# Kernel tuning notes

Hardware: AMD Instinct MI355X
Metric: run time of the kernel (lower is better)

## Reference

```python
import jax, jax.numpy as jnp
import numpy as np

BLOCK = 64          # block_dim
GAPS = (1, 64)      # block_dim**i for i in range(num_layers=2), input_dim=4096
N_BLOCKS = 64       # input_dim // block_dim
HID = 128           # 2 * block_dim (hidden_layers_ratio=[2])
BS = 8192
IN_DIM = 4096


def setup_inputs() -> dict:
    key = jax.random.key(0)
    kx, kw1, kw2 = jax.random.split(key, 3)
    x = jax.random.normal(kx, (BS, IN_DIM), dtype=jnp.float32)
    # one BlockResMLP per factorized layer: BlockLinear(64, 64, 128) -> ELU -> BlockLinear(64, 128, 64)
    w1 = jax.random.normal(kw1, (len(GAPS), N_BLOCKS, BLOCK, HID), dtype=jnp.float32) / np.sqrt(BLOCK)
    b1 = jnp.zeros((len(GAPS), N_BLOCKS, 1, HID), dtype=jnp.float32)
    w2 = jax.random.normal(kw2, (len(GAPS), N_BLOCKS, HID, BLOCK), dtype=jnp.float32) / np.sqrt(HID)
    b2 = jnp.zeros((len(GAPS), N_BLOCKS, 1, BLOCK), dtype=jnp.float32)
    return {"x": x, "w1": w1, "b1": b1, "w2": w2, "b2": b2}


def _facto(y, w1, b1, w2, b2):
    # BlockResMLP.forward: view(bs, n_blocks, BLOCK).transpose(0,1) -> batched block GEMMs -> residual
    bs = y.shape[0]
    z = y.reshape(bs, -1, BLOCK).transpose(1, 0, 2)              # (n_blocks, bs, BLOCK)
    h = jnp.einsum('nbd,nde->nbe', z, w1) + b1                   # BlockLinear 1 + bias
    h = jax.nn.elu(h)                                            # ELU (alpha=1)
    h = jnp.einsum('nbe,ned->nbd', h, w2) + b2                   # BlockLinear 2 + bias
    z = h + z                                                    # residual
    return z.transpose(1, 0, 2).reshape(bs, -1)


def reference(x, w1, b1, w2, b2):
    bs = x.shape[0]
    y = x
    for i, gap in enumerate(GAPS):
        # permutation shuffle: view(-1, BLOCK, gap).transpose(2,1).contiguous().view(bs,-1)
        y = y.reshape(-1, BLOCK, gap).transpose(0, 2, 1).reshape(bs, -1)
        y = _facto(y, w1[i], b1[i], w2[i], b2[i])
        # inverse shuffle: view(-1, gap, BLOCK).transpose(2,1)
        y = y.reshape(-1, gap, BLOCK).transpose(0, 2, 1).reshape(bs, -1)
    return y
```

## Files before the change

kernel.cpp:

```cpp
#include <hip/hip_runtime.h>


typedef short short8 __attribute__((ext_vector_type(8)));
typedef short short4v __attribute__((ext_vector_type(4)));
typedef float floatx4 __attribute__((ext_vector_type(4)));
typedef unsigned int uintx4 __attribute__((ext_vector_type(4)));

#define MFMA(A, B, C) __builtin_amdgcn_mfma_f32_16x16x32_bf16((A), (B), (C), 0, 0, 0)

__device__ __forceinline__ unsigned short bf16r(float f) {
  unsigned int u = __builtin_bit_cast(unsigned int, f);
  u += 0x7FFFu + ((u >> 16) & 1u);
  return (unsigned short)(u >> 16);
}
__device__ __forceinline__ float bf16f(unsigned short h) {
  unsigned int u = ((unsigned int)h) << 16;
  return __builtin_bit_cast(float, u);
}
__device__ __forceinline__ unsigned int pk2(float lo, float hi) {
  return (unsigned int)bf16r(lo) | ((unsigned int)bf16r(hi) << 16);
}
__device__ __forceinline__ float eluf(float v) {
  return v > 0.f ? v : (__expf(v) - 1.f);
}
__device__ __forceinline__ uint4 gather44(const short* A, const short* B, int s) {
  uint4 o;
  o.x = (unsigned int)(unsigned short)A[0 * s] |
        ((unsigned int)(unsigned short)A[1 * s] << 16);
  o.y = (unsigned int)(unsigned short)A[2 * s] |
        ((unsigned int)(unsigned short)A[3 * s] << 16);
  o.z = (unsigned int)(unsigned short)B[0 * s] |
        ((unsigned int)(unsigned short)B[1 * s] << 16);
  o.w = (unsigned int)(unsigned short)B[2 * s] |
        ((unsigned int)(unsigned short)B[3 * s] << 16);
  return o;
}

__global__ __launch_bounds__(256) void k0_prep(const float* __restrict__ w1,
                                               const float* __restrict__ w2,
                                               short* __restrict__ w1t,
                                               short* __restrict__ w2t) {
  __shared__ __align__(16) short T[128 * 72];
  const int t  = threadIdx.x;
  const int ln = blockIdx.x >> 1;
  if ((blockIdx.x & 1) == 0) {
    const bool pm = (ln >= 64);
    const float* src = w1 + (size_t)ln * 8192 + t * 32;
    const int d = t >> 2, e0 = (t & 3) * 32;
#pragma unroll
    for (int u = 0; u < 32; u += 2) {
      *(unsigned int*)&T[d * 136 + e0 + u] = pk2(src[u], src[u + 1]);
    }
    __syncthreads();
    const int e = t >> 1, d0 = (t & 1) * 32;
    short* dst = w1t + (size_t)ln * 8192 + e * 64 + d0;
#pragma unroll
    for (int k = 0; k < 4; ++k) {
      const int ta = d0 + (pm ? 4 * k : 8 * k);
      const int tb = d0 + (pm ? 16 + 4 * k : 8 * k + 4);
      *(uint4*)(dst + k * 8) = gather44(&T[ta * 136 + e], &T[tb * 136 + e], 136);
    }
  } else {
    const float* src = w2 + (size_t)ln * 8192 + t * 32;
    const int e = t >> 1, d0 = (t & 1) * 32;
#pragma unroll
    for (int u = 0; u < 32; u += 2) {
      *(unsigned int*)&T[e * 72 + d0 + u] = pk2(src[u], src[u + 1]);
    }
    __syncthreads();
    const int dp = t >> 2, e0 = (t & 3) * 32;
    short* dst = w2t + (size_t)ln * 8192 + dp * 128 + e0;
#pragma unroll
    for (int k = 0; k < 4; ++k) {
      const int ta = e0 + 4 * k;
      const int tb = e0 + 16 + 4 * k;
      *(uint4*)(dst + k * 8) = gather44(&T[ta * 72 + dp], &T[tb * 72 + dp], 72);
    }
  }
}

__global__ __launch_bounds__(256) void k1_layer0(
    const float* __restrict__ x,
    const short* __restrict__ w1t, const short* __restrict__ w2t,
    const float* __restrict__ b1,  const float* __restrict__ b2,
    short* __restrict__ y1) {
  const int tid  = threadIdx.x;
  const int lane = tid & 63;
  const int wv   = tid >> 6;
  const int il   = lane & 15;
  const int q    = lane >> 4;
  const int npair   = blockIdx.x & 31;
  const int rowtile = blockIdx.x >> 5;
  const int n  = npair * 2 + (wv & 1);
  const int r0 = rowtile * 64 + (wv >> 1) * 32;

  const short* w1n = w1t + (size_t)n * 8192;
  const short* w2n = w2t + (size_t)n * 8192;
  const float* b1n = b1 + n * 128;
  const float* b2n = b2 + n * 64;

  const floatx4 zero4 = {0.f, 0.f, 0.f, 0.f};
  short8 pbH;
#pragma unroll
  for (int v = 0; v < 8; ++v) pbH[v] = (v < 4 && il == q * 4 + v) ? (short)0x3F80 : (short)0;

  short8 a[2][2];
#pragma unroll
  for (int Mt = 0; Mt < 2; ++Mt) {
#pragma unroll
    for (int ks = 0; ks < 2; ++ks) {
      const float* xp = x + (size_t)(r0 + Mt * 16 + il) * 4096 + n * 64 + ks * 32 + q * 8;
      floatx4 f0 = *(const floatx4*)xp;
      floatx4 f1 = *(const floatx4*)(xp + 4);
      short8 t;
#pragma unroll
      for (int u = 0; u < 4; ++u) { t[u] = (short)bf16r(f0[u]); t[4 + u] = (short)bf16r(f1[u]); }
      a[ks][Mt] = t;
    }
  }

  floatx4 acc2[2][4] = {};
  for (int hh = 0; hh < 2; ++hh) {
    floatx4 acc1[2][4] = {};
#pragma unroll
    for (int ks = 0; ks < 2; ++ks) {
#pragma unroll
      for (int nt = 0; nt < 4; ++nt) {
        short8 b = *(const short8*)(w1n + (hh * 64 + nt * 16 + il) * 64 + ks * 32 + q * 8);
        acc1[0][nt] = MFMA(a[ks][0], b, acc1[0][nt]);
        acc1[1][nt] = MFMA(a[ks][1], b, acc1[1][nt]);
      }
    }
    uintx4 a2w[2][2];
#pragma unroll
    for (int Mt = 0; Mt < 2; ++Mt) {
#pragma unroll
      for (int nt = 0; nt < 4; ++nt) {
        const float bias = b1n[hh * 64 + nt * 16 + il];
        short8 ha = {(short)bf16r(eluf(acc1[Mt][nt][0] + bias)),
                     (short)bf16r(eluf(acc1[Mt][nt][1] + bias)),
                     (short)bf16r(eluf(acc1[Mt][nt][2] + bias)),
                     (short)bf16r(eluf(acc1[Mt][nt][3] + bias)),
                     0, 0, 0, 0};
        floatx4 hd = MFMA(ha, pbH, zero4);
        const int ks2l = nt >> 1;
        const int hf   = nt & 1;
        a2w[Mt][ks2l][hf * 2 + 0] = pk2(hd[0], hd[1]);
        a2w[Mt][ks2l][hf * 2 + 1] = pk2(hd[2], hd[3]);
      }
    }
#pragma unroll
    for (int ks2l = 0; ks2l < 2; ++ks2l) {
      short8 af0 = __builtin_bit_cast(short8, a2w[0][ks2l]);
      short8 af1 = __builtin_bit_cast(short8, a2w[1][ks2l]);
#pragma unroll
      for (int nt2 = 0; nt2 < 4; ++nt2) {
        short8 b = *(const short8*)(w2n + (nt2 * 16 + il) * 128 + hh * 64 + ks2l * 32 + q * 8);
        acc2[0][nt2] = MFMA(af0, b, acc2[0][nt2]);
        acc2[1][nt2] = MFMA(af1, b, acc2[1][nt2]);
      }
    }
  }

  short8 pb0, pb1;
#pragma unroll
  for (int v = 0; v < 8; ++v) {
    pb0[v] = (q * 8 + v == il)      ? (short)0x3F80 : (short)0;
    pb1[v] = (q * 8 + v == il + 16) ? (short)0x3F80 : (short)0;
  }
#pragma unroll
  for (int Mt = 0; Mt < 2; ++Mt) {
    const size_t nbase = ((size_t)((r0 + Mt * 16) >> 4) * 64 + n) * 64;
#pragma unroll
    for (int ks = 0; ks < 2; ++ks) {
      floatx4 xr[2];
      xr[0] = MFMA(a[ks][Mt], pb0, zero4);
      xr[1] = MFMA(a[ks][Mt], pb1, zero4);
#pragma unroll
      for (int h = 0; h < 2; ++h) {
        const int nt2 = ks * 2 + h;
        const int j = nt2 * 16 + il;
        const float bias = b2n[j];
        uint2 pk;
        pk.x = pk2(acc2[Mt][nt2][0] + bias + xr[h][0],
                   acc2[Mt][nt2][1] + bias + xr[h][1]);
        pk.y = pk2(acc2[Mt][nt2][2] + bias + xr[h][2],
                   acc2[Mt][nt2][3] + bias + xr[h][3]);
        *(uint2*)(y1 + (nbase + j) * 16 + q * 4) = pk;
      }
    }
  }
}

#define RSTR 1156
#define ISTR 18
__global__ __launch_bounds__(1024) void k2_layer1_out(
    const short* __restrict__ y1,
    const short* __restrict__ w1t, const short* __restrict__ w2t,
    const float* __restrict__ b1,  const float* __restrict__ b2,
    float* __restrict__ out) {
  __shared__ __align__(16) short yo[2][16 * RSTR];
  const int tid  = threadIdx.x;
  const int lane = tid & 63;
  const int wv   = tid >> 6;
  const int il   = lane & 15;
  const int q    = lane >> 4;
  const int rowband = blockIdx.x & 127;
  const int m0      = (blockIdx.x >> 7) * 16;
  const int m       = m0 + wv;

  short8 pb;
#pragma unroll
  for (int v = 0; v < 8; ++v) pb[v] = (v < 4 && il == q * 4 + v) ? (short)0x3F80 : (short)0;
  const floatx4 zero4 = {0.f, 0.f, 0.f, 0.f};

  const short* w1m = w1t + (size_t)(64 + m) * 8192;
  const short* w2m = w2t + (size_t)(64 + m) * 8192;
  const float* b1m = b1 + (64 + m) * 128;
  const float* b2m = b2 + (64 + m) * 64;

  short4v za[4][4];
#pragma unroll
  for (int g = 0; g < 4; ++g) {
    const int G = rowband * 4 + g;
#pragma unroll
    for (int nt = 0; nt < 4; ++nt)
      za[g][nt] = *(const short4v*)(y1 + ((size_t)(G * 64 + nt * 16 + il) * 64 + m) * 16 + q * 4);
  }

  const int fmq = tid & 3;
  const int fiw = (tid >> 2) & 63;
  const int frr = tid >> 8;

#pragma unroll
  for (int g = 0; g < 4; ++g) {
    floatx4 zd[4];
#pragma unroll
    for (int nt = 0; nt < 4; ++nt) {
      short8 az = {za[g][nt][0], za[g][nt][1], za[g][nt][2], za[g][nt][3], 0, 0, 0, 0};
      zd[nt] = MFMA(az, pb, zero4);
    }
    short8 at[2];
#pragma unroll
    for (int ks = 0; ks < 2; ++ks) {
      uintx4 w;
      w[0] = pk2(zd[2 * ks][0], zd[2 * ks][1]);
      w[1] = pk2(zd[2 * ks][2], zd[2 * ks][3]);
      w[2] = pk2(zd[2 * ks + 1][0], zd[2 * ks + 1][1]);
      w[3] = pk2(zd[2 * ks + 1][2], zd[2 * ks + 1][3]);
      at[ks] = __builtin_bit_cast(short8, w);
    }

    floatx4 acc2[4] = {};
    uintx4 a2w[4];
#pragma unroll
    for (int hh = 0; hh < 2; ++hh) {
      floatx4 acc1[4] = {};
#pragma unroll
      for (int ks = 0; ks < 2; ++ks)
#pragma unroll
        for (int nt = 0; nt < 4; ++nt) {
          short8 b = *(const short8*)(w1m + (hh * 64 + nt * 16 + il) * 64 + ks * 32 + q * 8);
          acc1[nt] = MFMA(at[ks], b, acc1[nt]);
        }
#pragma unroll
      for (int nt = 0; nt < 4; ++nt) {
        const float bias = b1m[hh * 64 + nt * 16 + il];
        short8 ha = {(short)bf16r(eluf(acc1[nt][0] + bias)),
                     (short)bf16r(eluf(acc1[nt][1] + bias)),
                     (short)bf16r(eluf(acc1[nt][2] + bias)),
                     (short)bf16r(eluf(acc1[nt][3] + bias)),
                     0, 0, 0, 0};
        floatx4 hd = MFMA(ha, pb, zero4);
        const int ks2 = hh * 2 + (nt >> 1);
        const int hf  = nt & 1;
        a2w[ks2][hf * 2 + 0] = pk2(hd[0], hd[1]);
        a2w[ks2][hf * 2 + 1] = pk2(hd[2], hd[3]);
      }
    }
#pragma unroll
    for (int ks2 = 0; ks2 < 4; ++ks2) {
      short8 af = __builtin_bit_cast(short8, a2w[ks2]);
#pragma unroll
      for (int nt2 = 0; nt2 < 4; ++nt2) {
        short8 b = *(const short8*)(w2m + (nt2 * 16 + il) * 128 + ks2 * 32 + q * 8);
        acc2[nt2] = MFMA(af, b, acc2[nt2]);
      }
    }
    short* yob = &yo[g & 1][0];
#pragma unroll
    for (int nt2 = 0; nt2 < 4; ++nt2) {
      const int i = nt2 * 16 + il;
      const float bias = b2m[i];
#pragma unroll
      for (int rg = 0; rg < 4; ++rg) {
        float val = acc2[nt2][rg] + bias + bf16f((unsigned short)za[g][nt2][rg]);
        yob[(q * 4 + rg) * RSTR + i * ISTR + wv] = (short)bf16r(val);
      }
    }
    __syncthreads();
    {
      const int G = rowband * 4 + g;
#pragma unroll
      for (int p = 0; p < 4; ++p) {
        const int r = p * 4 + frr;
        const short* yr = &yo[g & 1][r * RSTR + fiw * ISTR + fmq * 4];
        unsigned int w0 = *(const unsigned int*)(yr);
        unsigned int w1_ = *(const unsigned int*)(yr + 2);
        floatx4 vv = {bf16f((unsigned short)(w0 & 0xffffu)),
                      bf16f((unsigned short)(w0 >> 16)),
                      bf16f((unsigned short)(w1_ & 0xffffu)),
                      bf16f((unsigned short)(w1_ >> 16))};
        *(floatx4*)(out + (size_t)(G * 16 + r) * 4096 + fiw * 64 + m0 + fmq * 4) = vv;
      }
    }
  }
}

extern "C" void kernel_launch(void* const* d_in, const int* in_sizes, int n_in,
                              void* d_out, int out_size, void* d_ws, size_t ws_size,
                              hipStream_t stream) {
  const float* x  = (const float*)d_in[0];
  const float* w1 = (const float*)d_in[1];
  const float* b1 = (const float*)d_in[2];
  const float* w2 = (const float*)d_in[3];
  const float* b2 = (const float*)d_in[4];
  float* out = (float*)d_out;

  short* w1t = (short*)d_ws;
  short* w2t = w1t + (1u << 20);
  short* y1  = w2t + (1u << 20);

  hipLaunchKernelGGL(k0_prep,       dim3(256),  dim3(256),  0, stream, w1, w2, w1t, w2t);
  hipLaunchKernelGGL(k1_layer0,     dim3(4096), dim3(256),  0, stream, x, w1t, w2t, b1, b2, y1);
  hipLaunchKernelGGL(k2_layer1_out, dim3(512),  dim3(1024), 0, stream, y1, w1t, w2t, b1, b2, out);
}
```

Baseline: 481.7 us.

## Remap layer-1 output kernel so each block owns a full row group

The second-layer kernel now gives each block a single row group G and has every wave handle 2 of the 32 m-blocks per pass (two passes), instead of spreading 4 row groups across a 16-wide m slice. The LDS staging tile widens to 32 m-columns, so the output stores write 128-byte contiguous runs per row rather than 64-byte ones. This is meant to improve the coalescing of global writes. In exchange, each wave now cycles through more distinct weight matrices, which lowers weight reuse per block. The single LDS buffer also needs two barriers per pass.

```diff
diff --git a/kernel.cpp b/kernel.cpp
--- a/kernel.cpp
+++ b/kernel.cpp
@@ -192,128 +192,131 @@
   }
 }
 
-#define RSTR 1156
-#define ISTR 18
+#define RSTR 2308
+#define ISTR 36
 __global__ __launch_bounds__(1024) void k2_layer1_out(
     const short* __restrict__ y1,
     const short* __restrict__ w1t, const short* __restrict__ w2t,
     const float* __restrict__ b1,  const float* __restrict__ b2,
     float* __restrict__ out) {
-  __shared__ __align__(16) short yo[2][16 * RSTR];
+  __shared__ __align__(16) short yo[16 * RSTR];
   const int tid  = threadIdx.x;
   const int lane = tid & 63;
   const int wv   = tid >> 6;
   const int il   = lane & 15;
   const int q    = lane >> 4;
-  const int rowband = blockIdx.x & 127;
-  const int m0      = (blockIdx.x >> 7) * 16;
-  const int m       = m0 + wv;
+  const int G    = blockIdx.x;
 
   short8 pb;
 #pragma unroll
   for (int v = 0; v < 8; ++v) pb[v] = (v < 4 && il == q * 4 + v) ? (short)0x3F80 : (short)0;
   const floatx4 zero4 = {0.f, 0.f, 0.f, 0.f};
 
-  const short* w1m = w1t + (size_t)(64 + m) * 8192;
-  const short* w2m = w2t + (size_t)(64 + m) * 8192;
-  const float* b1m = b1 + (64 + m) * 128;
-  const float* b2m = b2 + (64 + m) * 64;
-
-  short4v za[4][4];
-#pragma unroll
-  for (int g = 0; g < 4; ++g) {
-    const int G = rowband * 4 + g;
-#pragma unroll
-    for (int nt = 0; nt < 4; ++nt)
-      za[g][nt] = *(const short4v*)(y1 + ((size_t)(G * 64 + nt * 16 + il) * 64 + m) * 16 + q * 4);
-  }
-
-  const int fmq = tid & 3;
-  const int fiw = (tid >> 2) & 63;
-  const int frr = tid >> 8;
-
-#pragma unroll
-  for (int g = 0; g < 4; ++g) {
-    floatx4 zd[4];
-#pragma unroll
-    for (int nt = 0; nt < 4; ++nt) {
-      short8 az = {za[g][nt][0], za[g][nt][1], za[g][nt][2], za[g][nt][3], 0, 0, 0, 0};
-      zd[nt] = MFMA(az, pb, zero4);
-    }
-    short8 at[2];
-#pragma unroll
-    for (int ks = 0; ks < 2; ++ks) {
-      uintx4 w;
-      w[0] = pk2(zd[2 * ks][0], zd[2 * ks][1]);
-      w[1] = pk2(zd[2 * ks][2], zd[2 * ks][3]);
-      w[2] = pk2(zd[2 * ks + 1][0], zd[2 * ks + 1][1]);
-      w[3] = pk2(zd[2 * ks + 1][2], zd[2 * ks + 1][3]);
-      at[ks] = __builtin_bit_cast(short8, w);
-    }
-
-    floatx4 acc2[4] = {};
-    uintx4 a2w[4];
-#pragma unroll
-    for (int hh = 0; hh < 2; ++hh) {
-      floatx4 acc1[4] = {};
-#pragma unroll
-      for (int ks = 0; ks < 2; ++ks)
+  short4v za[2][2][4];
+#pragma unroll
+  for (int p = 0; p < 2; ++p)
+#pragma unroll
+    for (int mi = 0; mi < 2; ++mi) {
+      const int m = p * 32 + wv * 2 + mi;
+#pragma unroll
+      for (int nt = 0; nt < 4; ++nt)
+        za[p][mi][nt] =
+            *(const short4v*)(y1 + ((size_t)(G * 64 + nt * 16 + il) * 64 + m) * 16 + q * 4);
+    }
+
+  const int fsub = tid & 7;
+  const int fic  = (tid >> 3) & 7;
+  const int fr   = tid >> 6;
+
+#pragma unroll
+  for (int p = 0; p < 2; ++p) {
+#pragma unroll
+    for (int mi = 0; mi < 2; ++mi) {
+      const int ml = wv * 2 + mi;
+      const int m  = p * 32 + ml;
+      const short* w1m = w1t + (size_t)(64 + m) * 8192;
+      const short* w2m = w2t + (size_t)(64 + m) * 8192;
+      const float* b1m = b1 + (64 + m) * 128;
+      const float* b2m = b2 + (64 + m) * 64;
+
+      floatx4 zd[4];
+#pragma unroll
+      for (int nt = 0; nt < 4; ++nt) {
+        short8 az = {za[p][mi][nt][0], za[p][mi][nt][1], za[p][mi][nt][2], za[p][mi][nt][3],
+                     0, 0, 0, 0};
+        zd[nt] = MFMA(az, pb, zero4);
+      }
+      short8 at[2];
+#pragma unroll
+      for (int ks = 0; ks < 2; ++ks) {
+        uintx4 w;
+        w[0] = pk2(zd[2 * ks][0], zd[2 * ks][1]);
+        w[1] = pk2(zd[2 * ks][2], zd[2 * ks][3]);
+        w[2] = pk2(zd[2 * ks + 1][0], zd[2 * ks + 1][1]);
+        w[3] = pk2(zd[2 * ks + 1][2], zd[2 * ks + 1][3]);
+        at[ks] = __builtin_bit_cast(short8, w);
+      }
+
+      floatx4 acc2[4] = {};
+      uintx4 a2w[4];
+#pragma unroll
+      for (int hh = 0; hh < 2; ++hh) {
+        floatx4 acc1[4] = {};
+#pragma unroll
+        for (int ks = 0; ks < 2; ++ks)
+#pragma unroll
+          for (int nt = 0; nt < 4; ++nt) {
+            short8 b = *(const short8*)(w1m + (hh * 64 + nt * 16 + il) * 64 + ks * 32 + q * 8);
+            acc1[nt] = MFMA(at[ks], b, acc1[nt]);
+          }
 #pragma unroll
         for (int nt = 0; nt < 4; ++nt) {
-          short8 b = *(const short8*)(w1m + (hh * 64 + nt * 16 + il) * 64 + ks * 32 + q * 8);
-          acc1[nt] = MFMA(at[ks], b, acc1[nt]);
+          const float bias = b1m[hh * 64 + nt * 16 + il];
+          short8 ha = {(short)bf16r(eluf(acc1[nt][0] + bias)),
+                       (short)bf16r(eluf(acc1[nt][1] + bias)),
+                       (short)bf16r(eluf(acc1[nt][2] + bias)),
+                       (short)bf16r(eluf(acc1[nt][3] + bias)),
+                       0, 0, 0, 0};
+          floatx4 hd = MFMA(ha, pb, zero4);
+          const int ks2 = hh * 2 + (nt >> 1);
+          const int hf  = nt & 1;
+          a2w[ks2][hf * 2 + 0] = pk2(hd[0], hd[1]);
+          a2w[ks2][hf * 2 + 1] = pk2(hd[2], hd[3]);
         }
-#pragma unroll
-      for (int nt = 0; nt < 4; ++nt) {
-        const float bias = b1m[hh * 64 + nt * 16 + il];
-        short8 ha = {(short)bf16r(eluf(acc1[nt][0] + bias)),
-                     (short)bf16r(eluf(acc1[nt][1] + bias)),
-                     (short)bf16r(eluf(acc1[nt][2] + bias)),
-                     (short)bf16r(eluf(acc1[nt][3] + bias)),
-                     0, 0, 0, 0};
-        floatx4 hd = MFMA(ha, pb, zero4);
-        const int ks2 = hh * 2 + (nt >> 1);
-        const int hf  = nt & 1;
-        a2w[ks2][hf * 2 + 0] = pk2(hd[0], hd[1]);
-        a2w[ks2][hf * 2 + 1] = pk2(hd[2], hd[3]);
-      }
-    }
-#pragma unroll
-    for (int ks2 = 0; ks2 < 4; ++ks2) {
-      short8 af = __builtin_bit_cast(short8, a2w[ks2]);
+      }
+#pragma unroll
+      for (int ks2 = 0; ks2 < 4; ++ks2) {
+        short8 af = __builtin_bit_cast(short8, a2w[ks2]);
+#pragma unroll
+        for (int nt2 = 0; nt2 < 4; ++nt2) {
+          short8 b = *(const short8*)(w2m + (nt2 * 16 + il) * 128 + ks2 * 32 + q * 8);
+          acc2[nt2] = MFMA(af, b, acc2[nt2]);
+        }
+      }
 #pragma unroll
       for (int nt2 = 0; nt2 < 4; ++nt2) {
-        short8 b = *(const short8*)(w2m + (nt2 * 16 + il) * 128 + ks2 * 32 + q * 8);
-        acc2[nt2] = MFMA(af, b, acc2[nt2]);
-      }
-    }
-    short* yob = &yo[g & 1][0];
-#pragma unroll
-    for (int nt2 = 0; nt2 < 4; ++nt2) {
-      const int i = nt2 * 16 + il;
-      const float bias = b2m[i];
-#pragma unroll
-      for (int rg = 0; rg < 4; ++rg) {
-        float val = acc2[nt2][rg] + bias + bf16f((unsigned short)za[g][nt2][rg]);
-        yob[(q * 4 + rg) * RSTR + i * ISTR + wv] = (short)bf16r(val);
+        const int i = nt2 * 16 + il;
+        const float bias = b2m[i];
+#pragma unroll
+        for (int rg = 0; rg < 4; ++rg) {
+          float val = acc2[nt2][rg] + bias + bf16f((unsigned short)za[p][mi][nt2][rg]);
+          yo[(q * 4 + rg) * RSTR + i * ISTR + ml] = (short)bf16r(val);
+        }
       }
     }
     __syncthreads();
-    {
-      const int G = rowband * 4 + g;
-#pragma unroll
-      for (int p = 0; p < 4; ++p) {
-        const int r = p * 4 + frr;
-        const short* yr = &yo[g & 1][r * RSTR + fiw * ISTR + fmq * 4];
-        unsigned int w0 = *(const unsigned int*)(yr);
-        unsigned int w1_ = *(const unsigned int*)(yr + 2);
-        floatx4 vv = {bf16f((unsigned short)(w0 & 0xffffu)),
-                      bf16f((unsigned short)(w0 >> 16)),
-                      bf16f((unsigned short)(w1_ & 0xffffu)),
-                      bf16f((unsigned short)(w1_ >> 16))};
-        *(floatx4*)(out + (size_t)(G * 16 + r) * 4096 + fiw * 64 + m0 + fmq * 4) = vv;
-      }
-    }
+#pragma unroll
+    for (int k = 0; k < 8; ++k) {
+      const int i = fic * 8 + k;
+      const short* yr = &yo[fr * RSTR + i * ISTR + fsub * 4];
+      uint2 w = *(const uint2*)yr;
+      floatx4 vv = {bf16f((unsigned short)(w.x & 0xffffu)),
+                    bf16f((unsigned short)(w.x >> 16)),
+                    bf16f((unsigned short)(w.y & 0xffffu)),
+                    bf16f((unsigned short)(w.y >> 16))};
+      *(floatx4*)(out + (size_t)(G * 16 + fr) * 4096 + i * 64 + p * 32 + fsub * 4) = vv;
+    }
+    __syncthreads();
   }
 }
 
```

Measured after the change: 451.8 us. -6.2%, faster.

## Fuse both factorized layers into one kernel with the intermediate kept in LDS

Applied to the files above, without the earlier changes.

Replaces the separate layer-0 and layer-1 kernels with one fused kernel. Each 1024-thread block owns 16 rows and computes all 64 layer-0 blocks into shared memory, syncs, runs all 64 layer-1 blocks from shared memory, then writes the fp32 output. This removes the bf16 intermediate round trip through global memory and one launch. In exchange it uses about 134KB of LDS per block, does 4 blocks per wave serially, and the final output stores are scalar (4-byte) writes.

```diff
diff --git a/kernel.cpp b/kernel.cpp
--- a/kernel.cpp
+++ b/kernel.cpp
@@ -79,166 +79,128 @@
   }
 }
 
-__global__ __launch_bounds__(256) void k1_layer0(
+#define NSTR 1048
+__global__ __launch_bounds__(1024, 4) void k12_fused(
     const float* __restrict__ x,
     const short* __restrict__ w1t, const short* __restrict__ w2t,
     const float* __restrict__ b1,  const float* __restrict__ b2,
-    short* __restrict__ y1) {
+    float* __restrict__ out) {
+  __shared__ __align__(16) short zL[64 * NSTR];
   const int tid  = threadIdx.x;
   const int lane = tid & 63;
   const int wv   = tid >> 6;
   const int il   = lane & 15;
   const int q    = lane >> 4;
-  const int npair   = blockIdx.x & 31;
-  const int rowtile = blockIdx.x >> 5;
-  const int n  = npair * 2 + (wv & 1);
-  const int r0 = rowtile * 64 + (wv >> 1) * 32;
-
-  const short* w1n = w1t + (size_t)n * 8192;
-  const short* w2n = w2t + (size_t)n * 8192;
-  const float* b1n = b1 + n * 128;
-  const float* b2n = b2 + n * 64;
+  const int R0   = blockIdx.x * 16;
 
   const floatx4 zero4 = {0.f, 0.f, 0.f, 0.f};
   short8 pbH;
 #pragma unroll
   for (int v = 0; v < 8; ++v) pbH[v] = (v < 4 && il == q * 4 + v) ? (short)0x3F80 : (short)0;
-
-  short8 a[2][2];
-#pragma unroll
-  for (int Mt = 0; Mt < 2; ++Mt) {
+  short8 pb0, pb1;
+#pragma unroll
+  for (int v = 0; v < 8; ++v) {
+    pb0[v] = (q * 8 + v == il)      ? (short)0x3F80 : (short)0;
+    pb1[v] = (q * 8 + v == il + 16) ? (short)0x3F80 : (short)0;
+  }
+
+  short8 a[4][2];
+#pragma unroll
+  for (int nn = 0; nn < 4; ++nn) {
 #pragma unroll
     for (int ks = 0; ks < 2; ++ks) {
-      const float* xp = x + (size_t)(r0 + Mt * 16 + il) * 4096 + n * 64 + ks * 32 + q * 8;
+      const float* xp = x + (size_t)(R0 + il) * 4096 + (wv * 4 + nn) * 64 + ks * 32 + q * 8;
       floatx4 f0 = *(const floatx4*)xp;
       floatx4 f1 = *(const floatx4*)(xp + 4);
       short8 t;
 #pragma unroll
       for (int u = 0; u < 4; ++u) { t[u] = (short)bf16r(f0[u]); t[4 + u] = (short)bf16r(f1[u]); }
-      a[ks][Mt] = t;
-    }
-  }
-
-  floatx4 acc2[2][4] = {};
-  for (int hh = 0; hh < 2; ++hh) {
-    floatx4 acc1[2][4] = {};
-#pragma unroll
-    for (int ks = 0; ks < 2; ++ks) {
-#pragma unroll
-      for (int nt = 0; nt < 4; ++nt) {
-        short8 b = *(const short8*)(w1n + (hh * 64 + nt * 16 + il) * 64 + ks * 32 + q * 8);
-        acc1[0][nt] = MFMA(a[ks][0], b, acc1[0][nt]);
-        acc1[1][nt] = MFMA(a[ks][1], b, acc1[1][nt]);
-      }
-    }
-    uintx4 a2w[2][2];
-#pragma unroll
-    for (int Mt = 0; Mt < 2; ++Mt) {
+      a[nn][ks] = t;
+    }
+  }
+
+#pragma unroll
+  for (int nn = 0; nn < 4; ++nn) {
+    const int n = wv * 4 + nn;
+    const short* w1n = w1t + (size_t)n * 8192;
+    const short* w2n = w2t + (size_t)n * 8192;
+    const float* b1n = b1 + n * 128;
+    const float* b2n = b2 + n * 64;
+
+    floatx4 acc2[4] = {};
+    for (int hh = 0; hh < 2; ++hh) {
+      floatx4 acc1[4] = {};
+#pragma unroll
+      for (int ks = 0; ks < 2; ++ks)
+#pragma unroll
+        for (int nt = 0; nt < 4; ++nt) {
+          short8 b = *(const short8*)(w1n + (hh * 64 + nt * 16 + il) * 64 + ks * 32 + q * 8);
+          acc1[nt] = MFMA(a[nn][ks], b, acc1[nt]);
+        }
+      uintx4 a2w[2];
 #pragma unroll
       for (int nt = 0; nt < 4; ++nt) {
         const float bias = b1n[hh * 64 + nt * 16 + il];
-        short8 ha = {(short)bf16r(eluf(acc1[Mt][nt][0] + bias)),
-                     (short)bf16r(eluf(acc1[Mt][nt][1] + bias)),
-                     (short)bf16r(eluf(acc1[Mt][nt][2] + bias)),
-                     (short)bf16r(eluf(acc1[Mt][nt][3] + bias)),
+        short8 ha = {(short)bf16r(eluf(acc1[nt][0] + bias)),
+                     (short)bf16r(eluf(acc1[nt][1] + bias)),
+                     (short)bf16r(eluf(acc1[nt][2] + bias)),
+                     (short)bf16r(eluf(acc1[nt][3] + bias)),
                      0, 0, 0, 0};
         floatx4 hd = MFMA(ha, pbH, zero4);
         const int ks2l = nt >> 1;
         const int hf   = nt & 1;
-        a2w[Mt][ks2l][hf * 2 + 0] = pk2(hd[0], hd[1]);
-        a2w[Mt][ks2l][hf * 2 + 1] = pk2(hd[2], hd[3]);
-      }
-    }
-#pragma unroll
-    for (int ks2l = 0; ks2l < 2; ++ks2l) {
-      short8 af0 = __builtin_bit_cast(short8, a2w[0][ks2l]);
-      short8 af1 = __builtin_bit_cast(short8, a2w[1][ks2l]);
-#pragma unroll
-      for (int nt2 = 0; nt2 < 4; ++nt2) {
-        short8 b = *(const short8*)(w2n + (nt2 * 16 + il) * 128 + hh * 64 + ks2l * 32 + q * 8);
-        acc2[0][nt2] = MFMA(af0, b, acc2[0][nt2]);
-        acc2[1][nt2] = MFMA(af1, b, acc2[1][nt2]);
-      }
-    }
-  }
-
-  short8 pb0, pb1;
-#pragma unroll
-  for (int v = 0; v < 8; ++v) {
-    pb0[v] = (q * 8 + v == il)      ? (short)0x3F80 : (short)0;
-    pb1[v] = (q * 8 + v == il + 16) ? (short)0x3F80 : (short)0;
-  }
-#pragma unroll
-  for (int Mt = 0; Mt < 2; ++Mt) {
-    const size_t nbase = ((size_t)((r0 + Mt * 16) >> 4) * 64 + n) * 64;
+        a2w[ks2l][hf * 2 + 0] = pk2(hd[0], hd[1]);
+        a2w[ks2l][hf * 2 + 1] = pk2(hd[2], hd[3]);
+      }
+#pragma unroll
+      for (int ks2l = 0; ks2l < 2; ++ks2l) {
+        short8 af = __builtin_bit_cast(short8, a2w[ks2l]);
+#pragma unroll
+        for (int nt2 = 0; nt2 < 4; ++nt2) {
+          short8 b = *(const short8*)(w2n + (nt2 * 16 + il) * 128 + hh * 64 + ks2l * 32 + q * 8);
+          acc2[nt2] = MFMA(af, b, acc2[nt2]);
+        }
+      }
+    }
 #pragma unroll
     for (int ks = 0; ks < 2; ++ks) {
       floatx4 xr[2];
-      xr[0] = MFMA(a[ks][Mt], pb0, zero4);
-      xr[1] = MFMA(a[ks][Mt], pb1, zero4);
+      xr[0] = MFMA(a[nn][ks], pb0, zero4);
+      xr[1] = MFMA(a[nn][ks], pb1, zero4);
 #pragma unroll
       for (int h = 0; h < 2; ++h) {
         const int nt2 = ks * 2 + h;
         const int j = nt2 * 16 + il;
         const float bias = b2n[j];
         uint2 pk;
-        pk.x = pk2(acc2[Mt][nt2][0] + bias + xr[h][0],
-                   acc2[Mt][nt2][1] + bias + xr[h][1]);
-        pk.y = pk2(acc2[Mt][nt2][2] + bias + xr[h][2],
-                   acc2[Mt][nt2][3] + bias + xr[h][3]);
-        *(uint2*)(y1 + (nbase + j) * 16 + q * 4) = pk;
-      }
-    }
-  }
-}
-
-#define RSTR 1156
-#define ISTR 18
-__global__ __launch_bounds__(1024) void k2_layer1_out(
-    const short* __restrict__ y1,
-    const short* __restrict__ w1t, const short* __restrict__ w2t,
-    const float* __restrict__ b1,  const float* __restrict__ b2,
-    float* __restrict__ out) {
-  __shared__ __align__(16) short yo[2][16 * RSTR];
-  const int tid  = threadIdx.x;
-  const int lane = tid & 63;
-  const int wv   = tid >> 6;
-  const int il   = lane & 15;
-  const int q    = lane >> 4;
-  const int rowband = blockIdx.x & 127;
-  const int m0      = (blockIdx.x >> 7) * 16;
-  const int m       = m0 + wv;
-
-  short8 pb;
-#pragma unroll
-  for (int v = 0; v < 8; ++v) pb[v] = (v < 4 && il == q * 4 + v) ? (short)0x3F80 : (short)0;
-  const floatx4 zero4 = {0.f, 0.f, 0.f, 0.f};
-
-  const short* w1m = w1t + (size_t)(64 + m) * 8192;
-  const short* w2m = w2t + (size_t)(64 + m) * 8192;
-  const float* b1m = b1 + (64 + m) * 128;
-  const float* b2m = b2 + (64 + m) * 64;
-
-  short4v za[4][4];
-#pragma unroll
-  for (int g = 0; g < 4; ++g) {
-    const int G = rowband * 4 + g;
+        pk.x = pk2(acc2[nt2][0] + bias + xr[h][0],
+                   acc2[nt2][1] + bias + xr[h][1]);
+        pk.y = pk2(acc2[nt2][2] + bias + xr[h][2],
+                   acc2[nt2][3] + bias + xr[h][3]);
+        *(uint2*)&zL[n * NSTR + j * 16 + q * 4] = pk;
+      }
+    }
+  }
+  __syncthreads();
+
+#pragma unroll
+  for (int mm = 0; mm < 4; ++mm) {
+    const int m = wv * 4 + mm;
+    const short* w1m = w1t + (size_t)(64 + m) * 8192;
+    const short* w2m = w2t + (size_t)(64 + m) * 8192;
+    const float* b1m = b1 + (64 + m) * 128;
+    const float* b2m = b2 + (64 + m) * 64;
+
+    short4v za[4];
 #pragma unroll
     for (int nt = 0; nt < 4; ++nt)
-      za[g][nt] = *(const short4v*)(y1 + ((size_t)(G * 64 + nt * 16 + il) * 64 + m) * 16 + q * 4);
-  }
-
-  const int fmq = tid & 3;
-  const int fiw = (tid >> 2) & 63;
-  const int frr = tid >> 8;
-
-#pragma unroll
-  for (int g = 0; g < 4; ++g) {
+      za[nt] = *(const short4v*)&zL[(nt * 16 + il) * NSTR + m * 16 + q * 4];
+
     floatx4 zd[4];
 #pragma unroll
     for (int nt = 0; nt < 4; ++nt) {
-      short8 az = {za[g][nt][0], za[g][nt][1], za[g][nt][2], za[g][nt][3], 0, 0, 0, 0};
-      zd[nt] = MFMA(az, pb, zero4);
+      short8 az = {za[nt][0], za[nt][1], za[nt][2], za[nt][3], 0, 0, 0, 0};
+      zd[nt] = MFMA(az, pbH, zero4);
     }
     short8 at[2];
 #pragma unroll
@@ -271,7 +233,7 @@
                      (short)bf16r(eluf(acc1[nt][2] + bias)),
                      (short)bf16r(eluf(acc1[nt][3] + bias)),
                      0, 0, 0, 0};
-        floatx4 hd = MFMA(ha, pb, zero4);
+        floatx4 hd = MFMA(ha, pbH, zero4);
         const int ks2 = hh * 2 + (nt >> 1);
         const int hf  = nt & 1;
         a2w[ks2][hf * 2 + 0] = pk2(hd[0], hd[1]);
@@ -287,33 +249,33 @@
         acc2[nt2] = MFMA(af, b, acc2[nt2]);
       }
     }
-    short* yob = &yo[g & 1][0];
 #pragma unroll
     for (int nt2 = 0; nt2 < 4; ++nt2) {
       const int i = nt2 * 16 + il;
       const float bias = b2m[i];
-#pragma unroll
-      for (int rg = 0; rg < 4; ++rg) {
-        float val = acc2[nt2][rg] + bias + bf16f((unsigned short)za[g][nt2][rg]);
-        yob[(q * 4 + rg) * RSTR + i * ISTR + wv] = (short)bf16r(val);
-      }
-    }
-    __syncthreads();
-    {
-      const int G = rowband * 4 + g;
-#pragma unroll
-      for (int p = 0; p < 4; ++p) {
-        const int r = p * 4 + frr;
-        const short* yr = &yo[g & 1][r * RSTR + fiw * ISTR + fmq * 4];
-        unsigned int w0 = *(const unsigned int*)(yr);
-        unsigned int w1_ = *(const unsigned int*)(yr + 2);
-        floatx4 vv = {bf16f((unsigned short)(w0 & 0xffffu)),
-                      bf16f((unsigned short)(w0 >> 16)),
-                      bf16f((unsigned short)(w1_ & 0xffffu)),
-                      bf16f((unsigned short)(w1_ >> 16))};
-        *(floatx4*)(out + (size_t)(G * 16 + r) * 4096 + fiw * 64 + m0 + fmq * 4) = vv;
-      }
-    }
+      uint2 pk;
+      pk.x = pk2(acc2[nt2][0] + bias + bf16f((unsigned short)za[nt2][0]),
+                 acc2[nt2][1] + bias + bf16f((unsigned short)za[nt2][1]));
+      pk.y = pk2(acc2[nt2][2] + bias + bf16f((unsigned short)za[nt2][2]),
+                 acc2[nt2][3] + bias + bf16f((unsigned short)za[nt2][3]));
+      *(uint2*)&zL[i * NSTR + m * 16 + q * 4] = pk;
+    }
+  }
+  __syncthreads();
+
+  const int fm = tid & 63;
+  const int fb = tid >> 6;
+#pragma unroll
+  for (int k = 0; k < 16; ++k) {
+    const int iq = fb * 16 + k;
+    const int i  = iq >> 2;
+    const int fq = iq & 3;
+    uint2 z = *(const uint2*)&zL[i * NSTR + fm * 16 + fq * 4];
+    const size_t ob = (size_t)(R0 + fq * 4) * 4096 + i * 64 + fm;
+    out[ob]         = bf16f((unsigned short)(z.x & 0xffffu));
+    out[ob + 4096]  = bf16f((unsigned short)(z.x >> 16));
+    out[ob + 8192]  = bf16f((unsigned short)(z.y & 0xffffu));
+    out[ob + 12288] = bf16f((unsigned short)(z.y >> 16));
   }
 }
 
@@ -329,9 +291,7 @@
 
   short* w1t = (short*)d_ws;
   short* w2t = w1t + (1u << 20);
-  short* y1  = w2t + (1u << 20);
-
-  hipLaunchKernelGGL(k0_prep,       dim3(256),  dim3(256),  0, stream, w1, w2, w1t, w2t);
-  hipLaunchKernelGGL(k1_layer0,     dim3(4096), dim3(256),  0, stream, x, w1t, w2t, b1, b2, y1);
-  hipLaunchKernelGGL(k2_layer1_out, dim3(512),  dim3(1024), 0, stream, y1, w1t, w2t, b1, b2, out);
-}
+
+  hipLaunchKernelGGL(k0_prep,   dim3(256), dim3(256),  0, stream, w1, w2, w1t, w2t);
+  hipLaunchKernelGGL(k12_fused, dim3(512), dim3(1024), 0, stream, x, w1t, w2t, b1, b2, out);
+}
```

New measurement: 481.3 us. Within noise of the previous version (-0.1%).
